# Kernel optimization log

Hardware: AMD Instinct MI355X
Metric: run time of the kernel (lower is better)

Reference implementation:

```python
import jax, jax.numpy as jnp
import numpy as np

NUM_WIRES = 12
NUM_LAYERS = 4
NUM_OUTPUTS = 4
BATCH = 1024
DIM = 2 ** NUM_WIRES


def _apply_1q(psi, U, w):
    # psi: (B, 2**n) complex64; U: (2,2) shared or (B,2,2) per-sample; wire 0 = most significant.
    B = psi.shape[0]
    L = 2 ** w
    R = DIM // (2 * L)
    psi = psi.reshape(B, L, 2, R)
    if U.ndim == 2:
        psi = jnp.einsum('ij,bljr->blir', U, psi)
    else:
        psi = jnp.einsum('bij,bljr->blir', U, psi)
    return psi.reshape(B, DIM)


def _cnot(psi, c, t):
    # CNOT(control=c, target=t): flip target amplitudes in the control=1 half.
    B = psi.shape[0]
    psi = psi.reshape((B,) + (2,) * NUM_WIRES)
    a0 = jax.lax.index_in_dim(psi, 0, c + 1, keepdims=True)
    a1 = jax.lax.index_in_dim(psi, 1, c + 1, keepdims=True)
    a1 = jnp.flip(a1, axis=t + 1)
    psi = jnp.concatenate([a0, a1], axis=c + 1)
    return psi.reshape(B, DIM)


def _rot(phi, theta, omega):
    # PennyLane Rot(phi, theta, omega) = RZ(omega) @ RY(theta) @ RZ(phi)
    c = jnp.cos(theta / 2)
    s = jnp.sin(theta / 2)
    u00 = jnp.exp(-0.5j * (phi + omega)) * c
    u01 = -jnp.exp(0.5j * (phi - omega)) * s
    u10 = jnp.exp(-0.5j * (phi - omega)) * s
    u11 = jnp.exp(0.5j * (phi + omega)) * c
    return jnp.stack([jnp.stack([u00, u01]), jnp.stack([u10, u11])]).astype(jnp.complex64)


def _circuit(inputs, weights):
    B = inputs.shape[0]
    psi = jnp.zeros((B, DIM), jnp.complex64).at[:, 0].set(1.0)
    # AngleEmbedding with rotation 'Y': RY(pi/2 * x_w) on wire w (per-sample angles)
    theta = (jnp.pi / 2) * inputs  # (B, n)
    c = jnp.cos(theta / 2)
    s = jnp.sin(theta / 2)
    for w in range(NUM_WIRES):
        U = jnp.stack([jnp.stack([c[:, w], -s[:, w]], -1),
                       jnp.stack([s[:, w], c[:, w]], -1)], -2).astype(jnp.complex64)  # (B,2,2)
        psi = _apply_1q(psi, U, w)
    # StronglyEntanglingLayers: Rot on every wire, then ring of CNOTs with range r
    for l in range(NUM_LAYERS):
        for w in range(NUM_WIRES):
            psi = _apply_1q(psi, _rot(weights[l, w, 0], weights[l, w, 1], weights[l, w, 2]), w)
        r = (l % (NUM_WIRES - 1)) + 1
        for w in range(NUM_WIRES):
            psi = _cnot(psi, w, (w + r) % NUM_WIRES)
    # expval(PauliZ) on the first NUM_OUTPUTS wires
    probs = jnp.abs(psi) ** 2  # (B, DIM) float32
    idx = jnp.arange(DIM)
    shifts = NUM_WIRES - 1 - jnp.arange(NUM_OUTPUTS)
    signs = (1.0 - 2.0 * ((idx[None, :] >> shifts[:, None]) & 1)).astype(probs.dtype)  # (NOUT, DIM)
    return probs @ signs.T  # (B, NUM_OUTPUTS)


def setup_inputs() -> dict:
    key = jax.random.key(0)
    k1, k2 = jax.random.split(key)
    inputs = jax.random.uniform(k1, (BATCH, NUM_WIRES), jnp.float32, -1.0, 1.0)
    weights = jax.random.uniform(k2, (NUM_LAYERS, NUM_WIRES, 3), jnp.float32, 0.0, 2.0 * np.pi)
    return {"inputs": inputs, "weights": weights}


def reference(inputs, weights):
    return _circuit(inputs, weights)
```

## Files before the change

### kernel.cpp

```cpp
#include <hip/hip_runtime.h>
#include <hip/hip_bf16.h>

#define NW 12
#define DIM 4096
#define NL 4
#define NGATE 48
#define NOUT 4
#define TPB 512

typedef float f32x2 __attribute__((ext_vector_type(2)));
typedef float f32x4 __attribute__((ext_vector_type(4)));
typedef unsigned u32x4 __attribute__((ext_vector_type(4)));
typedef short short8 __attribute__((ext_vector_type(8)));

constexpr int pcnt(unsigned x){ return __builtin_popcount(x); }
constexpr int msbp(unsigned x){ return x ? 31-__builtin_clz(x) : -1; }
constexpr unsigned ring_fwd(unsigned x,int r){
  for(int w=0;w<NW;++w){ int c=NW-1-w,t=NW-1-((w+r)%NW); x^=((x>>c)&1u)<<t; } return x;
}
constexpr unsigned ring_rev(unsigned x,int r){
  for(int w=NW-1;w>=0;--w){ int c=NW-1-w,t=NW-1-((w+r)%NW); x^=((x>>c)&1u)<<t; } return x;
}
struct Mat { unsigned col[12]; };
constexpr unsigned apply_cols(const Mat&M, unsigned v){
  unsigned r=0; for(int j=0;j<12;++j) if((v>>j)&1u) r^=M.col[j]; return r;
}
constexpr unsigned apply_rows(const unsigned* rows, unsigned v){
  unsigned r=0; for(int i=0;i<12;++i) r|=(unsigned)(pcnt(rows[i]&v)&1)<<i; return r;
}
constexpr bool invert_rows(const Mat&M, unsigned* ri_out){
  unsigned rb[12]={}, ri[12]={};
  for(int i=0;i<12;++i){ unsigned r=0; for(int j=0;j<12;++j) r|=((M.col[j]>>i)&1u)<<j; rb[i]=r; ri[i]=1u<<i; }
  for(int c=0;c<12;++c){
    int piv=-1; for(int r=c;r<12;++r) if((rb[r]>>c)&1u){piv=r;break;}
    if(piv<0) return false;
    unsigned t=rb[c]; rb[c]=rb[piv]; rb[piv]=t; t=ri[c]; ri[c]=ri[piv]; ri[piv]=t;
    for(int r=0;r<12;++r) if(r!=c&&((rb[r]>>c)&1u)){ rb[r]^=rb[c]; ri[r]^=ri[c]; }
  }
  for(int i=0;i<12;++i) ri_out[i]=ri[i];
  return true;
}
constexpr int nullspace4(const unsigned* A0, unsigned* out){
  unsigned A[4]={}; for(int i=0;i<4;++i) A[i]=A0[i];
  int rank=0; int pivc[4]={-1,-1,-1,-1};
  for(int c=0;c<12&&rank<4;++c){
    int piv=-1; for(int r=rank;r<4;++r) if((A[r]>>c)&1u){piv=r;break;}
    if(piv<0) continue;
    unsigned t=A[rank];A[rank]=A[piv];A[piv]=t;
    for(int r=0;r<4;++r) if(r!=rank&&((A[r]>>c)&1u)) A[r]^=A[rank];
    pivc[rank]=c; ++rank;
  }
  if(rank!=4) return -1;
  bool ispiv[12]={};
  for(int r=0;r<4;++r) ispiv[pivc[r]]=true;
  int cnt=0;
  for(int f=0;f<12;++f) if(!ispiv[f]){
    unsigned v=1u<<f;
    for(int r=0;r<4;++r) if((A[r]>>f)&1u) v|=1u<<pivc[r];
    out[cnt++]=v;
  }
  return cnt;
}
struct Ech { unsigned r[12]; int lead[12]; int n; };
constexpr unsigned ech_red(const Ech&e, unsigned v){
  int mv=msbp(v);
  for(int i=0;i<e.n&&v;++i) if(e.lead[i]==mv){ v^=e.r[i]; mv=msbp(v); }
  return v;
}
constexpr void ech_add(Ech&e, unsigned v){
  int l=msbp(v); int pos=e.n;
  while(pos>0&&e.lead[pos-1]<l){ e.r[pos]=e.r[pos-1]; e.lead[pos]=e.lead[pos-1]; --pos; }
  e.r[pos]=v; e.lead[pos]=l; e.n+=1;
}

struct Circ {
  unsigned M[NL][12]; unsigned RM[NL][12]; unsigned MR[NOUT];
};
constexpr Circ make_circ(){
  Circ C{};
  unsigned cols[12]={}, icols[12]={};
  for(int p=0;p<12;++p){ cols[p]=1u<<p; icols[p]=1u<<p; }
  for(int l=0;l<NL;++l){
    for(int w=0;w<NW;++w){
      int p=NW-1-w;
      C.M[l][w]=icols[p];
      unsigned r=0; for(int j=0;j<12;++j) r|=((cols[j]>>p)&1u)<<j;
      C.RM[l][w]=r;
    }
    int rr=(l%(NW-1))+1;
    for(int j=0;j<12;++j) cols[j]=ring_fwd(cols[j],rr);
    unsigned nic[12]={};
    for(int p=0;p<12;++p){
      unsigned y=ring_rev(1u<<p,rr), v=0;
      for(int q=0;q<12;++q) if((y>>q)&1u) v^=icols[q];
      nic[p]=v;
    }
    for(int p=0;p<12;++p) icols[p]=nic[p];
  }
  for(int o=0;o<NOUT;++o){
    int p=NW-1-o; unsigned r=0;
    for(int j=0;j<12;++j) r|=((cols[j]>>p)&1u)<<j;
    C.MR[o]=r;
  }
  return C;
}

constexpr unsigned amap(unsigned v){ return (v>>8)*2048u + (v&255u)*8u; }

struct Plan2 {
  unsigned SCOLt[8];
  unsigned SK16[16];
  unsigned TM;
  unsigned WBC[12][8], WOFF[12][16];
  unsigned RBC[12][8], ROFF[12][16];
  unsigned SRt[NOUT], KP[NOUT];
  bool ok;
};

constexpr Plan2 make_plan2(){
  Plan2 P{}; P.ok=true;
  constexpr Circ C = make_circ();
  const int SIGl[8] = {0,1,2,3,10,11,6,7};
  Mat Bprev{}; for(int j=0;j<12;++j) Bprev.col[j]=1u<<j;
  for(int g=0; g<12; ++g){
    int l=g/3, j0=(g%3)*4;
    unsigned mi[4]={}, rmi[4]={};
    for(int i=0;i<4;++i){ mi[i]=C.M[l][j0+i]; rmi[i]=C.RM[l][j0+i]; }
    unsigned u[8]={};
    if(nullspace4(rmi,u)!=8){ P.ok=false; return P; }
    unsigned binv[12]={};
    if(!invert_rows(Bprev,binv)){ P.ok=false; return P; }
    for(int s=0;s<8;++s) u[s]=apply_rows(binv,u[s]);
    Mat Bg{};
    for(int j=0;j<8;++j) Bg.col[j]=apply_cols(Bprev,u[j]);
    for(int i=0;i<4;++i) Bg.col[8+i]=mi[i];
    unsigned tinv[12]={};
    if(!invert_rows(Bg,tinv)){ P.ok=false; return P; }
    for(int i=0;i<4;++i)
      for(int j=0;j<12;++j){
        int want=(j==8+i)?1:0;
        if((pcnt(Bg.col[j]&rmi[i])&1)!=want){ P.ok=false; return P; }
      }
    if(g==0){
      for(int j=0;j<8;++j) P.SCOLt[j]=Bg.col[SIGl[j]];
      for(int idx=0;idx<16;++idx){
        unsigned v=0;
        if((idx>>2)&1) v^=Bg.col[4];
        if((idx>>2)&2) v^=Bg.col[5];
        if(idx&1) v^=Bg.col[8];
        if(idx&2) v^=Bg.col[9];
        P.SK16[idx]=v; P.TM|=v;
      }
    } else {
      unsigned rk[4]={};
      for(int i=0;i<4;++i){
        rk[i]=apply_rows(binv,mi[i]);
        if(apply_cols(Bprev,rk[i])!=mi[i]){ P.ok=false; return P; }
      }
      unsigned s2b[6]={u[0],u[1],u[2],u[3],rk[2],rk[3]};
      unsigned rows[12]={}; int nr=0;
      Ech P1{},P2{},ER{};
      for(int pick=0;pick<4;++pick){
        unsigned fx=0, fy=0;
        const int b1s[6]={0,1,2,3,10,11};
        for(int ii=0;ii<6;++ii){
          unsigned f=1u<<b1s[ii];
          unsigned p1=(f&15u)|(((f>>10)&3u)<<4);
          if(ech_red(P1,p1)){ fx=f; break; }
        }
        for(int bb=0;bb<12;++bb){
          unsigned f=1u<<bb, p2=0;
          for(int i2=0;i2<6;++i2) p2|=(unsigned)(pcnt(f&s2b[i2])&1)<<i2;
          if(ech_red(P2,p2)){ fy=f; break; }
        }
        if(!fx||!fy){ P.ok=false; return P; }
        unsigned cand[3]={fx,fy,fx^fy};
        unsigned chosen=0, cp1=0, cp2=0;
        for(int ci=0; ci<3 && !chosen; ++ci){
          unsigned f=cand[ci];
          unsigned p1=(f&15u)|(((f>>10)&3u)<<4);
          unsigned p2=0; for(int i2=0;i2<6;++i2) p2|=(unsigned)(pcnt(f&s2b[i2])&1)<<i2;
          if(ech_red(P1,p1)&&ech_red(P2,p2)){ chosen=f; cp1=p1; cp2=p2; }
        }
        if(!chosen){ P.ok=false; return P; }
        { unsigned v1=ech_red(P1,cp1); ech_add(P1,v1); }
        { unsigned v2=ech_red(P2,cp2); ech_add(P2,v2); }
        { unsigned vr=ech_red(ER,chosen); if(!vr){ P.ok=false; return P; } ech_add(ER,vr); }
        rows[nr++]=chosen;
      }
      for(int bb=0;bb<12 && nr<12;++bb){
        unsigned vr=ech_red(ER,1u<<bb); if(!vr) continue;
        ech_add(ER,vr); rows[nr++]=1u<<bb;
      }
      if(nr!=12){ P.ok=false; return P; }
      unsigned PhiCol[12]={};
      for(int j=0;j<12;++j){
        unsigned v=0;
        for(int i=0;i<12;++i) v|=(unsigned)((rows[i]>>j)&1u)<<i;
        PhiCol[j]=v;
      }
      unsigned PhiM[12]={};
      for(int j=0;j<12;++j){
        unsigned src=(j<8)? u[j] : rk[j-8];
        unsigned v=0;
        for(int q2=0;q2<12;++q2) if((src>>q2)&1u) v^=PhiCol[q2];
        PhiM[j]=v;
      }
      for(int j=0;j<8;++j){
        P.WBC[g][j]=amap(PhiCol[SIGl[j]]);
        P.RBC[g][j]=amap(PhiM[SIGl[j]]);
      }
      for(int idx=0;idx<16;++idx){
        unsigned wv=0, rv=0;
        if((idx>>2)&1){ wv^=PhiCol[4]; rv^=PhiM[4]; }
        if((idx>>2)&2){ wv^=PhiCol[5]; rv^=PhiM[5]; }
        if(idx&1){ wv^=PhiCol[8]; rv^=PhiM[8]; }
        if(idx&2){ wv^=PhiCol[9]; rv^=PhiM[9]; }
        P.WOFF[g][idx]=amap(wv); P.ROFF[g][idx]=amap(rv);
      }
    }
    Bprev=Bg;
  }
  for(int o=0;o<NOUT;++o){
    unsigned sr=0;
    for(int j=0;j<12;++j) sr|=(unsigned)(pcnt(Bprev.col[j]&C.MR[o])&1)<<j;
    unsigned srt=0;
    const int SIGl2[8] = {0,1,2,3,10,11,6,7};
    for(int j=0;j<8;++j) srt|=((sr>>SIGl2[j])&1u)<<j;
    P.SRt[o]=srt;
    unsigned kp=0;
    for(int idx=0;idx<16;++idx){
      int T=idx>>2, q=idx&3;
      unsigned bit=(((sr>>4)&1u)&(unsigned)(T&1))^(((sr>>5)&1u)&(unsigned)((T>>1)&1))
                  ^(((sr>>8)&1u)&(unsigned)(q&1))^(((sr>>9)&1u)&(unsigned)((q>>1)&1));
      kp|=bit<<idx;
    }
    P.KP[o]=kp;
  }
  return P;
}

constexpr Plan2 PL2C = make_plan2();
static_assert(PL2C.ok, "plan2 failed");
__device__ constexpr Plan2 PL2 = PL2C;

__device__ __forceinline__ void gate_coeffs(const float* __restrict__ wts, int gi, float* o){
  const float* w = wts + gi*3;
  float st,ct;  sincosf(0.5f*w[1],&st,&ct);
  float sap,cap; sincosf(0.5f*(w[0]+w[2]),&sap,&cap);
  float sam,cam; sincosf(0.5f*(w[0]-w[2]),&sam,&cam);
  o[0]= cap*ct; o[1]=-sap*ct;
  o[2]=-cam*st; o[3]=-sam*st;
  o[4]= cam*st; o[5]=-sam*st;
  o[6]= cap*ct; o[7]= sap*ct;
}
__device__ __forceinline__ unsigned cvtpk(float a, float b){
  unsigned r; asm("v_cvt_pk_bf16_f32 %0, %1, %2" : "=v"(r) : "v"(a), "v"(b)); return r;
}
__device__ __forceinline__ void split2(float x, float& hf, float& lf){
  __hip_bfloat16 hb = __float2bfloat16(x);
  hf = __bfloat162float(hb);
  lf = x - hf;
}
__device__ __forceinline__ void pkhl(float x0, float x1, unsigned& hw_out, unsigned& lw_out){
  unsigned hw = cvtpk(x0, x1);
  float h0 = __uint_as_float(hw << 16);
  float h1 = __uint_as_float(hw & 0xffff0000u);
  lw_out = cvtpk(x0 - h0, x1 - h1);
  hw_out = hw;
}

__global__ void coeff2_kernel(const float* __restrict__ wts, unsigned short* __restrict__ gfrag){
  const int g = blockIdx.x;
  const int tid = threadIdx.x;
  const int m = tid & 15, rp = tid >> 4;
  const int s = rp >> 1, reg = rp & 1;
  const int r0 = 4*s + 2*reg, r1 = r0 + 1;
  const int l = g/3, j0 = (g%3)*4;
  float ur0=1.f, ui0=0.f, ur1=1.f, ui1=0.f;
  #pragma unroll
  for(int i=0;i<4;++i){
    float o[8]; gate_coeffs(wts, l*NW + j0 + i, o);
    int mb=(m>>i)&1, rb0=(r0>>i)&1, rb1=(r1>>i)&1;
    float er=o[(mb*2+rb0)*2], ei=o[(mb*2+rb0)*2+1];
    float tr=ur0*er-ui0*ei, ti=ur0*ei+ui0*er; ur0=tr; ui0=ti;
    er=o[(mb*2+rb1)*2]; ei=o[(mb*2+rb1)*2+1];
    tr=ur1*er-ui1*ei; ti=ur1*ei+ui1*er; ur1=tr; ui1=ti;
  }
  float ur0h,ur0l,ur1h,ur1l, ui0h,ui0l,ui1h,ui1l;
  split2(ur0,ur0h,ur0l); split2(ur1,ur1h,ur1l);
  split2(ui0,ui0h,ui0l); split2(ui1,ui1h,ui1l);
  unsigned Urh=cvtpk(ur0h,ur1h), Url=cvtpk(ur0l,ur1l);
  unsigned Uih=cvtpk(ui0h,ui1h), Uil=cvtpk(ui0l,ui1l);
  unsigned nUih=Uih^0x80008000u, nUil=Uil^0x80008000u;
  const int lane = s*16 + m;
  unsigned p0[6]={Urh,Url,Uih,Uil,nUih,nUil};
  unsigned p1[6]={Url,Urh,Uil,Uih,nUil,nUih};
  #pragma unroll
  for(int f=0; f<6; ++f){
    unsigned* fp = (unsigned*)((char*)gfrag + ((size_t)((g*6+f)*64 + lane))*16);
    fp[reg] = p0[f];
    fp[2+reg] = p1[f];
  }
}

#define LUT_BYTES (11*64*4)
__global__ __launch_bounds__(TPB,8)
void vqc_mfma(const float* __restrict__ inp, const unsigned short* __restrict__ gfrag,
              float* __restrict__ out){
  __shared__ __align__(16) char smem[2*DIM*8 + LUT_BYTES];
  __shared__ float cs2[2][NW], ss2[2][NW];
  __shared__ float red[8][NOUT];
  unsigned* blut = (unsigned*)(smem + 2*DIM*8);
  const int t = threadIdx.x, b = blockIdx.x, l = t&63;
  const int tt = t & 255, smp = t >> 8;
  char* ampc = smem + smp*(DIM*8);
  if(tt < NW){
    float x = inp[(b*2+smp)*NW+tt];
    float s,c; sincosf(0.78539816339744830962f*x,&s,&c);
    cs2[smp][tt]=c; ss2[smp][tt]=s;
  }
  for(int e=t; e<11*64; e+=TPB){
    int gg=(e>>6)+1, idx=e&63;
    int kind=idx>>4, nib=idx&15;
    unsigned v=0;
    #pragma unroll
    for(int j=0;j<4;++j){
      if((nib>>j)&1){
        int jj = j + ((kind&1)?4:0);
        v ^= (kind<2)? PL2.WBC[gg][jj] : PL2.RBC[gg][jj];
      }
    }
    blut[e]=v;
  }
  __syncthreads();
  float ctm[12], stm[12];
  #pragma unroll
  for(int p=0;p<12;++p){ ctm[p]=cs2[smp][11-p]; stm[p]=ss2[smp][11-p]; }
  unsigned sigb=0;
  #pragma unroll
  for(int j=0;j<8;++j) sigb ^= ((tt>>j)&1u)? PL2.SCOLt[j] : 0u;
  float pbase=1.f;
  #pragma unroll
  for(int p=0;p<12;++p)
    if(!((PL2C.TM>>p)&1u))
      pbase *= ((sigb>>p)&1u)? stm[p] : ctm[p];

  short8 AF[6];
  #pragma unroll
  for(int f=0; f<6; ++f)
    AF[f] = *(const short8*)((const char*)gfrag + ((size_t)(f*64 + l))*16);

  f32x4 Cr[4], Ci[4];
  #pragma unroll 1
  for(int g=0; g<12; ++g){
    unsigned rbase=0;
    if(g>0){
      const unsigned* bl = blut + (g-1)*64;
      unsigned wbase = bl[tt&15] ^ bl[16 + (tt>>4)];
      rbase          = bl[32 + (tt&15)] ^ bl[48 + (tt>>4)];
      __syncthreads();
      #pragma unroll
      for(int idx=0; idx<16; ++idx){
        const int T=idx>>2, q=idx&3;
        *(float2*)(ampc + (wbase ^ PL2.WOFF[g][idx])) = make_float2(Cr[T][q], Ci[T][q]);
      }
      __syncthreads();
    }
    #pragma unroll
    for(int T=0;T<4;++T){
      float2 v0,v1,v2,v3;
      if(g==0){
        float vv[4];
        #pragma unroll
        for(int rq=0;rq<4;++rq){
          unsigned sig = sigb ^ PL2.SK16[T*4+rq];
          float pk=pbase;
          #pragma unroll
          for(int p=0;p<12;++p)
            if((PL2C.TM>>p)&1u)
              pk *= ((sig>>p)&1u)? stm[p] : ctm[p];
          vv[rq]=pk;
        }
        v0=make_float2(vv[0],0.f); v1=make_float2(vv[1],0.f);
        v2=make_float2(vv[2],0.f); v3=make_float2(vv[3],0.f);
      } else {
        v0 = *(const float2*)(ampc + (rbase ^ PL2.ROFF[g][T*4+0]));
        v1 = *(const float2*)(ampc + (rbase ^ PL2.ROFF[g][T*4+1]));
        v2 = *(const float2*)(ampc + (rbase ^ PL2.ROFF[g][T*4+2]));
        v3 = *(const float2*)(ampc + (rbase ^ PL2.ROFF[g][T*4+3]));
      }
      unsigned h0,l0,h1,l1;
      pkhl(v0.x, v1.x, h0, l0);
      pkhl(v2.x, v3.x, h1, l1);
      u32x4 bu; bu.x=h0; bu.y=h1; bu.z=l0; bu.w=l1;
      short8 Br = __builtin_bit_cast(short8, bu);
      pkhl(v0.y, v1.y, h0, l0);
      pkhl(v2.y, v3.y, h1, l1);
      u32x4 cu; cu.x=h0; cu.y=h1; cu.z=l0; cu.w=l1;
      short8 Bi = __builtin_bit_cast(short8, cu);
      const f32x4 z = {0.f,0.f,0.f,0.f};
      f32x4 cr = __builtin_amdgcn_mfma_f32_16x16x32_bf16(AF[0], Br, z, 0,0,0);
      cr = __builtin_amdgcn_mfma_f32_16x16x32_bf16(AF[1], Br, cr, 0,0,0);
      cr = __builtin_amdgcn_mfma_f32_16x16x32_bf16(AF[4], Bi, cr, 0,0,0);
      cr = __builtin_amdgcn_mfma_f32_16x16x32_bf16(AF[5], Bi, cr, 0,0,0);
      f32x4 ci = __builtin_amdgcn_mfma_f32_16x16x32_bf16(AF[2], Br, z, 0,0,0);
      ci = __builtin_amdgcn_mfma_f32_16x16x32_bf16(AF[3], Br, ci, 0,0,0);
      ci = __builtin_amdgcn_mfma_f32_16x16x32_bf16(AF[0], Bi, ci, 0,0,0);
      ci = __builtin_amdgcn_mfma_f32_16x16x32_bf16(AF[1], Bi, ci, 0,0,0);
      Cr[T]=cr; Ci[T]=ci;
    }
    if(g<11){
      #pragma unroll
      for(int f=0; f<6; ++f)
        AF[f] = *(const short8*)((const char*)gfrag + ((size_t)(((g+1)*6+f)*64 + l))*16);
    }
  }
  float acc[NOUT]={0.f,0.f,0.f,0.f};
  float sg[NOUT];
  #pragma unroll
  for(int o=0;o<NOUT;++o)
    sg[o] = (__popc((unsigned)tt & PL2.SRt[o])&1)? -1.f : 1.f;
  #pragma unroll
  for(int idx=0; idx<16; ++idx){
    const int T=idx>>2, q=idx&3;
    float pr = Cr[T][q]*Cr[T][q] + Ci[T][q]*Ci[T][q];
    #pragma unroll
    for(int o=0;o<NOUT;++o){
      const bool kp = (PL2C.KP[o]>>idx)&1;
      float f = sg[o]*pr;
      acc[o] += kp? -f : f;
    }
  }
  #pragma unroll
  for(int o=0;o<NOUT;++o)
    #pragma unroll
    for(int off=32; off>0; off>>=1)
      acc[o] += __shfl_down(acc[o], off);
  __syncthreads();
  const int wv=t>>6, ln=t&63;
  if(ln==0){
    #pragma unroll
    for(int o=0;o<NOUT;++o) red[wv][o]=acc[o];
  }
  __syncthreads();
  if(tt<NOUT){
    const int w0 = smp*4;
    out[(b*2+smp)*NOUT+tt] = red[w0][tt]+red[w0+1][tt]+red[w0+2][tt]+red[w0+3][tt];
  }
}

extern "C" void kernel_launch(void* const* d_in, const int* in_sizes, int n_in,
                              void* d_out, int out_size, void* d_ws, size_t ws_size,
                              hipStream_t stream) {
  const float* inp=(const float*)d_in[0];
  const float* wts=(const float*)d_in[1];
  float* outp=(float*)d_out;
  const int B = in_sizes[0]/NW;
  unsigned short* gfrag=(unsigned short*)d_ws;
  coeff2_kernel<<<12,128,0,stream>>>(wts,gfrag);
  vqc_mfma<<<B/2,TPB,0,stream>>>(inp,gfrag,outp);
}
```

Before: 42.02 us.

## Process one sample per 256-thread block and peel the first gate iteration

Each block now simulates a single sample with 256 threads instead of two samples with 512 threads, so block-wide barriers cover half as many waves and twice as many blocks are launched. The first gate group, which builds amplitudes from the embedding, is peeled out of the loop, removing a per-iteration branch. The write and read bit-index lookup tables are interleaved into one uint2 table so a single load returns both. The MFMA sequences are wrapped in s_setprio raises. The scalar scratch arrays are aliased into the amplitude buffer, which is safe only because they are read before that buffer is first written or written after it is last read.

```diff
diff --git a/kernel.cpp b/kernel.cpp
--- a/kernel.cpp
+++ b/kernel.cpp
@@ -6,7 +6,7 @@
 #define NL 4
 #define NGATE 48
 #define NOUT 4
-#define TPB 512
+#define TPB 256
 
 typedef float f32x2 __attribute__((ext_vector_type(2)));
 typedef float f32x4 __attribute__((ext_vector_type(4)));
@@ -270,6 +270,30 @@
   hw_out = hw;
 }
 
+__device__ __forceinline__ void do_mfma_T(const float2& v0, const float2& v1,
+                                          const float2& v2, const float2& v3,
+                                          const short8* AF, f32x4& cr_o, f32x4& ci_o){
+  unsigned h0,l0,h1,l1;
+  pkhl(v0.x, v1.x, h0, l0);
+  pkhl(v2.x, v3.x, h1, l1);
+  u32x4 bu; bu.x=h0; bu.y=h1; bu.z=l0; bu.w=l1;
+  short8 Br = __builtin_bit_cast(short8, bu);
+  pkhl(v0.y, v1.y, h0, l0);
+  pkhl(v2.y, v3.y, h1, l1);
+  u32x4 cu; cu.x=h0; cu.y=h1; cu.z=l0; cu.w=l1;
+  short8 Bi = __builtin_bit_cast(short8, cu);
+  const f32x4 z = {0.f,0.f,0.f,0.f};
+  f32x4 cr = __builtin_amdgcn_mfma_f32_16x16x32_bf16(AF[0], Br, z, 0,0,0);
+  cr = __builtin_amdgcn_mfma_f32_16x16x32_bf16(AF[1], Br, cr, 0,0,0);
+  cr = __builtin_amdgcn_mfma_f32_16x16x32_bf16(AF[4], Bi, cr, 0,0,0);
+  cr = __builtin_amdgcn_mfma_f32_16x16x32_bf16(AF[5], Bi, cr, 0,0,0);
+  f32x4 ci = __builtin_amdgcn_mfma_f32_16x16x32_bf16(AF[2], Br, z, 0,0,0);
+  ci = __builtin_amdgcn_mfma_f32_16x16x32_bf16(AF[3], Br, ci, 0,0,0);
+  ci = __builtin_amdgcn_mfma_f32_16x16x32_bf16(AF[0], Bi, ci, 0,0,0);
+  ci = __builtin_amdgcn_mfma_f32_16x16x32_bf16(AF[1], Bi, ci, 0,0,0);
+  cr_o = cr; ci_o = ci;
+}
+
 __global__ void coeff2_kernel(const float* __restrict__ wts, unsigned short* __restrict__ gfrag){
   const int g = blockIdx.x;
   const int tid = threadIdx.x;
@@ -304,42 +328,41 @@
   }
 }
 
-#define LUT_BYTES (11*64*4)
-__global__ __launch_bounds__(TPB,8)
+#define LUT_BYTES (11*32*8)
+__global__ __launch_bounds__(TPB,4)
 void vqc_mfma(const float* __restrict__ inp, const unsigned short* __restrict__ gfrag,
               float* __restrict__ out){
-  __shared__ __align__(16) char smem[2*DIM*8 + LUT_BYTES];
-  __shared__ float cs2[2][NW], ss2[2][NW];
-  __shared__ float red[8][NOUT];
-  unsigned* blut = (unsigned*)(smem + 2*DIM*8);
+  __shared__ __align__(16) char smem[DIM*8 + LUT_BYTES];
+  float* cs = (float*)smem; float* ss = cs+NW; float* red = cs+2*NW;
+  char* ampc = smem;
+  uint2* blut = (uint2*)(smem + DIM*8);
   const int t = threadIdx.x, b = blockIdx.x, l = t&63;
-  const int tt = t & 255, smp = t >> 8;
-  char* ampc = smem + smp*(DIM*8);
-  if(tt < NW){
-    float x = inp[(b*2+smp)*NW+tt];
+  if(t < NW){
+    float x = inp[b*NW+t];
     float s,c; sincosf(0.78539816339744830962f*x,&s,&c);
-    cs2[smp][tt]=c; ss2[smp][tt]=s;
-  }
-  for(int e=t; e<11*64; e+=TPB){
-    int gg=(e>>6)+1, idx=e&63;
-    int kind=idx>>4, nib=idx&15;
-    unsigned v=0;
+    cs[t]=c; ss[t]=s;
+  }
+  for(int e=t; e<11*32; e+=TPB){
+    int gg=(e>>5)+1, idx=e&31;
+    int hi=idx>>4, nib=idx&15;
+    unsigned wv=0, rv=0;
     #pragma unroll
     for(int j=0;j<4;++j){
       if((nib>>j)&1){
-        int jj = j + ((kind&1)?4:0);
-        v ^= (kind<2)? PL2.WBC[gg][jj] : PL2.RBC[gg][jj];
-      }
-    }
-    blut[e]=v;
+        int jj = j + (hi?4:0);
+        wv ^= PL2.WBC[gg][jj];
+        rv ^= PL2.RBC[gg][jj];
+      }
+    }
+    blut[e]=make_uint2(wv,rv);
   }
   __syncthreads();
   float ctm[12], stm[12];
   #pragma unroll
-  for(int p=0;p<12;++p){ ctm[p]=cs2[smp][11-p]; stm[p]=ss2[smp][11-p]; }
+  for(int p=0;p<12;++p){ ctm[p]=cs[11-p]; stm[p]=ss[11-p]; }
   unsigned sigb=0;
   #pragma unroll
-  for(int j=0;j<8;++j) sigb ^= ((tt>>j)&1u)? PL2.SCOLt[j] : 0u;
+  for(int j=0;j<8;++j) sigb ^= ((t>>j)&1u)? PL2.SCOLt[j] : 0u;
   float pbase=1.f;
   #pragma unroll
   for(int p=0;p<12;++p)
@@ -352,63 +375,55 @@
     AF[f] = *(const short8*)((const char*)gfrag + ((size_t)(f*64 + l))*16);
 
   f32x4 Cr[4], Ci[4];
+
+  {
+    #pragma unroll
+    for(int T=0;T<4;++T){
+      float vv[4];
+      #pragma unroll
+      for(int rq=0;rq<4;++rq){
+        unsigned sig = sigb ^ PL2.SK16[T*4+rq];
+        float pk=pbase;
+        #pragma unroll
+        for(int p=0;p<12;++p)
+          if((PL2C.TM>>p)&1u)
+            pk *= ((sig>>p)&1u)? stm[p] : ctm[p];
+        vv[rq]=pk;
+      }
+      float2 v0=make_float2(vv[0],0.f), v1=make_float2(vv[1],0.f);
+      float2 v2=make_float2(vv[2],0.f), v3=make_float2(vv[3],0.f);
+      __builtin_amdgcn_s_setprio(1);
+      do_mfma_T(v0,v1,v2,v3, AF, Cr[T], Ci[T]);
+      __builtin_amdgcn_s_setprio(0);
+    }
+    #pragma unroll
+    for(int f=0; f<6; ++f)
+      AF[f] = *(const short8*)((const char*)gfrag + ((size_t)((6+f)*64 + l))*16);
+  }
+
   #pragma unroll 1
-  for(int g=0; g<12; ++g){
-    unsigned rbase=0;
-    if(g>0){
-      const unsigned* bl = blut + (g-1)*64;
-      unsigned wbase = bl[tt&15] ^ bl[16 + (tt>>4)];
-      rbase          = bl[32 + (tt&15)] ^ bl[48 + (tt>>4)];
-      __syncthreads();
-      #pragma unroll
-      for(int idx=0; idx<16; ++idx){
-        const int T=idx>>2, q=idx&3;
-        *(float2*)(ampc + (wbase ^ PL2.WOFF[g][idx])) = make_float2(Cr[T][q], Ci[T][q]);
-      }
-      __syncthreads();
-    }
+  for(int g=1; g<12; ++g){
+    const uint2* bl = blut + (g-1)*32;
+    uint2 lo = bl[t&15];
+    uint2 hi = bl[16 + (t>>4)];
+    unsigned wbase = lo.x ^ hi.x;
+    unsigned rbase = lo.y ^ hi.y;
+    __syncthreads();
+    #pragma unroll
+    for(int idx=0; idx<16; ++idx){
+      const int T=idx>>2, q=idx&3;
+      *(float2*)(ampc + (wbase ^ PL2.WOFF[g][idx])) = make_float2(Cr[T][q], Ci[T][q]);
+    }
+    __syncthreads();
     #pragma unroll
     for(int T=0;T<4;++T){
-      float2 v0,v1,v2,v3;
-      if(g==0){
-        float vv[4];
-        #pragma unroll
-        for(int rq=0;rq<4;++rq){
-          unsigned sig = sigb ^ PL2.SK16[T*4+rq];
-          float pk=pbase;
-          #pragma unroll
-          for(int p=0;p<12;++p)
-            if((PL2C.TM>>p)&1u)
-              pk *= ((sig>>p)&1u)? stm[p] : ctm[p];
-          vv[rq]=pk;
-        }
-        v0=make_float2(vv[0],0.f); v1=make_float2(vv[1],0.f);
-        v2=make_float2(vv[2],0.f); v3=make_float2(vv[3],0.f);
-      } else {
-        v0 = *(const float2*)(ampc + (rbase ^ PL2.ROFF[g][T*4+0]));
-        v1 = *(const float2*)(ampc + (rbase ^ PL2.ROFF[g][T*4+1]));
-        v2 = *(const float2*)(ampc + (rbase ^ PL2.ROFF[g][T*4+2]));
-        v3 = *(const float2*)(ampc + (rbase ^ PL2.ROFF[g][T*4+3]));
-      }
-      unsigned h0,l0,h1,l1;
-      pkhl(v0.x, v1.x, h0, l0);
-      pkhl(v2.x, v3.x, h1, l1);
-      u32x4 bu; bu.x=h0; bu.y=h1; bu.z=l0; bu.w=l1;
-      short8 Br = __builtin_bit_cast(short8, bu);
-      pkhl(v0.y, v1.y, h0, l0);
-      pkhl(v2.y, v3.y, h1, l1);
-      u32x4 cu; cu.x=h0; cu.y=h1; cu.z=l0; cu.w=l1;
-      short8 Bi = __builtin_bit_cast(short8, cu);
-      const f32x4 z = {0.f,0.f,0.f,0.f};
-      f32x4 cr = __builtin_amdgcn_mfma_f32_16x16x32_bf16(AF[0], Br, z, 0,0,0);
-      cr = __builtin_amdgcn_mfma_f32_16x16x32_bf16(AF[1], Br, cr, 0,0,0);
-      cr = __builtin_amdgcn_mfma_f32_16x16x32_bf16(AF[4], Bi, cr, 0,0,0);
-      cr = __builtin_amdgcn_mfma_f32_16x16x32_bf16(AF[5], Bi, cr, 0,0,0);
-      f32x4 ci = __builtin_amdgcn_mfma_f32_16x16x32_bf16(AF[2], Br, z, 0,0,0);
-      ci = __builtin_amdgcn_mfma_f32_16x16x32_bf16(AF[3], Br, ci, 0,0,0);
-      ci = __builtin_amdgcn_mfma_f32_16x16x32_bf16(AF[0], Bi, ci, 0,0,0);
-      ci = __builtin_amdgcn_mfma_f32_16x16x32_bf16(AF[1], Bi, ci, 0,0,0);
-      Cr[T]=cr; Ci[T]=ci;
+      float2 v0 = *(const float2*)(ampc + (rbase ^ PL2.ROFF[g][T*4+0]));
+      float2 v1 = *(const float2*)(ampc + (rbase ^ PL2.ROFF[g][T*4+1]));
+      float2 v2 = *(const float2*)(ampc + (rbase ^ PL2.ROFF[g][T*4+2]));
+      float2 v3 = *(const float2*)(ampc + (rbase ^ PL2.ROFF[g][T*4+3]));
+      __builtin_amdgcn_s_setprio(1);
+      do_mfma_T(v0,v1,v2,v3, AF, Cr[T], Ci[T]);
+      __builtin_amdgcn_s_setprio(0);
     }
     if(g<11){
       #pragma unroll
@@ -416,11 +431,12 @@
         AF[f] = *(const short8*)((const char*)gfrag + ((size_t)(((g+1)*6+f)*64 + l))*16);
     }
   }
+
   float acc[NOUT]={0.f,0.f,0.f,0.f};
   float sg[NOUT];
   #pragma unroll
   for(int o=0;o<NOUT;++o)
-    sg[o] = (__popc((unsigned)tt & PL2.SRt[o])&1)? -1.f : 1.f;
+    sg[o] = (__popc((unsigned)t & PL2.SRt[o])&1)? -1.f : 1.f;
   #pragma unroll
   for(int idx=0; idx<16; ++idx){
     const int T=idx>>2, q=idx&3;
@@ -441,13 +457,11 @@
   const int wv=t>>6, ln=t&63;
   if(ln==0){
     #pragma unroll
-    for(int o=0;o<NOUT;++o) red[wv][o]=acc[o];
+    for(int o=0;o<NOUT;++o) red[wv*NOUT+o]=acc[o];
   }
   __syncthreads();
-  if(tt<NOUT){
-    const int w0 = smp*4;
-    out[(b*2+smp)*NOUT+tt] = red[w0][tt]+red[w0+1][tt]+red[w0+2][tt]+red[w0+3][tt];
-  }
+  if(t<NOUT)
+    out[b*NOUT+t] = red[0*NOUT+t]+red[1*NOUT+t]+red[2*NOUT+t]+red[3*NOUT+t];
 }
 
 extern "C" void kernel_launch(void* const* d_in, const int* in_sizes, int n_in,
@@ -459,5 +473,5 @@
   const int B = in_sizes[0]/NW;
   unsigned short* gfrag=(unsigned short*)d_ws;
   coeff2_kernel<<<12,128,0,stream>>>(wts,gfrag);
-  vqc_mfma<<<B/2,TPB,0,stream>>>(inp,gfrag,outp);
-}
+  vqc_mfma<<<B,TPB,0,stream>>>(inp,gfrag,outp);
+}
```

New measurement: 39.74 us, median of 2. -5.4%, faster.
